# Optimization experiments

Measured on AMD Instinct MI355X. Metric: run time of the kernel, lower is better.

Reference implementation:

```python
import jax, jax.numpy as jnp
import numpy as np

B, S, D, H = 4, 2048, 1024, 16
DK = D // H

def setup_inputs() -> dict:
    key = jax.random.key(0)
    ks = jax.random.split(key, 12)
    def lin(kk, fan_in):
        bound = 1.0 / np.sqrt(fan_in)
        kw, kb = jax.random.split(kk)
        W = jax.random.uniform(kw, (fan_in, D), jnp.float32, -bound, bound)
        b = jax.random.uniform(kb, (D,), jnp.float32, -bound, bound)
        return W, b
    Wq, bq = lin(ks[0], D)
    Wk, bk = lin(ks[1], D)
    Wv, bv = lin(ks[2], D)
    Wo, bo = lin(ks[3], D)
    q = jax.random.normal(ks[4], (B, S, D), jnp.float32)
    k = jax.random.normal(ks[5], (B, S, D), jnp.float32)
    v = jax.random.normal(ks[6], (B, S, D), jnp.float32)
    mask = jnp.tril(jnp.ones((S, S), jnp.int32))[None, None]  # [1,1,S,S] causal
    return {"q": q, "k": k, "v": v, "mask": mask,
            "Wq": Wq, "bq": bq, "Wk": Wk, "bk": bk,
            "Wv": Wv, "bv": bv, "Wo": Wo, "bo": bo}

def reference(q, k, v, mask, Wq, bq, Wk, bk, Wv, bv, Wo, bo):
    Bq, Sq, _ = q.shape
    # projections
    Q = (q @ Wq + bq).reshape(Bq, Sq, H, DK).transpose(0, 2, 1, 3)  # [B,H,S,DK]
    K = (k @ Wk + bk).reshape(Bq, Sq, H, DK).transpose(0, 2, 1, 3)
    V = (v @ Wv + bv).reshape(Bq, Sq, H, DK).transpose(0, 2, 1, 3)
    scale = 1.0 / jnp.sqrt(jnp.float32(DK))
    scores = jnp.einsum('bhqd,bhkd->bhqk', Q, K) * scale  # [B,H,S,S]
    scores = jnp.where(mask == 0, jnp.float32(-jnp.inf), scores)
    attn = jax.nn.softmax(scores, axis=-1)
    # dropout p=0.0 -> identity
    x = jnp.einsum('bhqk,bhkd->bhqd', attn, V)  # [B,H,S,DK]
    x = x.transpose(0, 2, 1, 3).reshape(Bq, Sq, D)
    return x @ Wo + bo
```

## Files before the change

### kernel.cpp

```cpp
#include <hip/hip_runtime.h>

typedef unsigned short u16;
typedef __attribute__((ext_vector_type(4))) float f32x4;
typedef __attribute__((ext_vector_type(8))) __bf16 bf16x8;
typedef __attribute__((ext_vector_type(4))) unsigned int u32x4;

#define S_LEN 2048
#define D_DIM 1024
#define N_HEADS 16
#define DK 64
#define B_SZ 4

__device__ __forceinline__ u16 f2bf(float f) {
  unsigned int u = __float_as_uint(f);
  unsigned int r = (u + 0x7FFFu + ((u >> 16) & 1u)) >> 16;
  return (u16)r;
}
__device__ __forceinline__ unsigned int cvtpk(float a, float b) {
  unsigned int r;
  asm("v_cvt_pk_bf16_f32 %0, %1, %2" : "=v"(r) : "v"(a), "v"(b));
  return r;
}
__device__ __forceinline__ f32x4 mfma16(u32x4 a, u32x4 b, f32x4 c) {
  return __builtin_amdgcn_mfma_f32_16x16x32_bf16(
      __builtin_bit_cast(bf16x8, a), __builtin_bit_cast(bf16x8, b), c, 0, 0, 0);
}
__device__ __forceinline__ void gload_lds16(const void* g, void* l) {
  __builtin_amdgcn_global_load_lds(
      (const __attribute__((address_space(1))) void*)g,
      (__attribute__((address_space(3))) void*)l, 16, 0, 0);
}

__global__ __launch_bounds__(256) void transpose_all(
    const float* __restrict__ W0, const float* __restrict__ W1,
    const float* __restrict__ W2, const float* __restrict__ W3,
    u16* __restrict__ T0, u16* __restrict__ T1,
    u16* __restrict__ T2, u16* __restrict__ T3) {
  __shared__ float tb[32][33];
  const int z = blockIdx.z;
  const float* W = (z == 0) ? W0 : (z == 1) ? W1 : (z == 2) ? W2 : W3;
  u16* WT = (z == 0) ? T0 : (z == 1) ? T1 : (z == 2) ? T2 : T3;
  const int tx = threadIdx.x & 31;
  const int ty0 = (threadIdx.x >> 5) << 2;
  const int bn = blockIdx.x << 5;
  const int bk = blockIdx.y << 5;
#pragma unroll
  for (int i = 0; i < 4; ++i)
    tb[ty0 + i][tx] = W[(size_t)(bk + ty0 + i) * D_DIM + bn + tx];
  __syncthreads();
#pragma unroll
  for (int i = 0; i < 4; ++i)
    WT[(size_t)(bn + ty0 + i) * D_DIM + bk + tx] = f2bf(tb[tx][ty0 + i]);
}

template <int AF32, int BPRE>
__global__ __launch_bounds__(256) void gemm_xw(const void* __restrict__ Av,
                                               const void* __restrict__ Bv,
                                               const float* __restrict__ bias,
                                               void* __restrict__ dstv,
                                               const int epi, const float osc) {
  __shared__ __align__(16) u16 As[128 * 40];
  __shared__ __align__(16) u16 Bs[128 * 40];
  const int tid = threadIdx.x;
  const int lane = tid & 63;
  const int wid = tid >> 6;
  const int wr = wid >> 1, wc = wid & 1;
  const int lr = lane & 15, lg = lane >> 4;
  const int m0 = blockIdx.x * 128;
  const int n0 = blockIdx.y * 128;

  const float* Xf = (const float*)Av;
  const u16* Xh = (const u16*)Av;
  const float* Wf = (const float*)Bv;
  const u16* WT = (const u16*)Bv;

  f32x4 acc[4][4];
#pragma unroll
  for (int i = 0; i < 4; ++i)
#pragma unroll
    for (int j = 0; j < 4; ++j) acc[i][j] = (f32x4){0.f, 0.f, 0.f, 0.f};

  const int srow = tid >> 2;
  const int sko = (tid & 3) << 3;
  const int glr = lane >> 2;
  const int glc = ((lane & 3) ^ (glr & 3)) << 3;

  for (int k0 = 0; k0 < D_DIM; k0 += 32) {
    __syncthreads();
    if (AF32) {
#pragma unroll
      for (int i = 0; i < 2; ++i) {
        const int row = srow + i * 64;
        const float* src = &Xf[(size_t)(m0 + row) * D_DIM + k0 + sko];
        f32x4 a0 = *(const f32x4*)src;
        f32x4 a1 = *(const f32x4*)(src + 4);
        u32x4 pk = (u32x4){cvtpk(a0[0], a0[1]), cvtpk(a0[2], a0[3]),
                           cvtpk(a1[0], a1[1]), cvtpk(a1[2], a1[3])};
        *(u32x4*)&As[row * 40 + sko] = pk;
      }
    } else {
#pragma unroll
      for (int j = 0; j < 2; ++j) {
        const int rbase = wid * 32 + j * 16;
        gload_lds16(&Xh[(size_t)(m0 + rbase + glr) * D_DIM + k0 + glc],
                    &As[rbase * 32]);
      }
    }
    if (BPRE) {
#pragma unroll
      for (int j = 0; j < 2; ++j) {
        const int rbase = wid * 32 + j * 16;
        gload_lds16(&WT[(size_t)(n0 + rbase + glr) * D_DIM + k0 + glc],
                    &Bs[rbase * 32]);
      }
    } else {
#pragma unroll
      for (int i = 0; i < 2; ++i) {
        const int s = tid + (i << 8);
        const int kr = s >> 4;
        const int mN = s & 15;
        const int nc = mN << 3;
        const float* src = &Wf[(size_t)(k0 + kr) * D_DIM + n0 + nc];
        f32x4 w0 = *(const f32x4*)src;
        f32x4 w1 = *(const f32x4*)(src + 4);
        const int cb = (((kr >> 3) ^ (mN & 3)) << 3) + (kr & 7);
#pragma unroll
        for (int j = 0; j < 4; ++j) {
          Bs[(nc + j) * 40 + cb] = f2bf(w0[j]);
          Bs[(nc + 4 + j) * 40 + cb] = f2bf(w1[j]);
        }
      }
    }
    __syncthreads();
    u32x4 af[4], bfr[4];
#pragma unroll
    for (int mi = 0; mi < 4; ++mi) {
      const int row = wr * 64 + mi * 16 + lr;
      if (AF32)
        af[mi] = *(const u32x4*)&As[row * 40 + lg * 8];
      else
        af[mi] = *(const u32x4*)&As[row * 32 + ((lg ^ (row & 3)) << 3)];
    }
#pragma unroll
    for (int ni = 0; ni < 4; ++ni) {
      const int row = wc * 64 + ni * 16 + lr;
      if (BPRE)
        bfr[ni] = *(const u32x4*)&Bs[row * 32 + ((lg ^ (row & 3)) << 3)];
      else
        bfr[ni] = *(const u32x4*)&Bs[row * 40 + ((lg ^ ((row >> 3) & 3)) << 3)];
    }
#pragma unroll
    for (int mi = 0; mi < 4; ++mi)
#pragma unroll
      for (int ni = 0; ni < 4; ++ni)
        acc[mi][ni] = mfma16(af[mi], bfr[ni], acc[mi][ni]);
  }

#pragma unroll
  for (int ni = 0; ni < 4; ++ni) {
    const int n = n0 + wc * 64 + ni * 16 + lr;
    const float bv = bias[n];
#pragma unroll
    for (int mi = 0; mi < 4; ++mi) {
      const int mb = m0 + wr * 64 + mi * 16 + lg * 4;
      float o[4];
#pragma unroll
      for (int r = 0; r < 4; ++r) o[r] = (acc[mi][ni][r] + bv) * osc;
      if (epi == 0) {
#pragma unroll
        for (int r = 0; r < 4; ++r)
          ((float*)dstv)[(size_t)(mb + r) * D_DIM + n] = o[r];
      } else {
        const unsigned int w0 = cvtpk(o[0], o[1]);
        const unsigned int w1 = cvtpk(o[2], o[3]);
        const int bb = mb >> 11, ss = mb & (S_LEN - 1);
        const int hh = n >> 6, dd = n & (DK - 1);
        if (epi == 2) {
          union { unsigned int u[2]; unsigned long long q; } pk;
          pk.u[0] = w0; pk.u[1] = w1;
          *(unsigned long long*)&((u16*)dstv)[((size_t)((bb * N_HEADS + hh) * DK + dd)) * S_LEN + ss] = pk.q;
        } else {
          u16* dp = &((u16*)dstv)[(((size_t)(bb * N_HEADS + hh) * S_LEN) + ss) * DK + dd];
          dp[0] = (u16)w0;
          dp[DK] = (u16)(w0 >> 16);
          dp[2 * DK] = (u16)w1;
          dp[3 * DK] = (u16)(w1 >> 16);
        }
      }
    }
  }
}

__global__ __launch_bounds__(256) void attn_kernel(const u16* __restrict__ Qb,
                                                   const u16* __restrict__ Kb,
                                                   const u16* __restrict__ VTb,
                                                   u16* __restrict__ Xb) {
  __shared__ __align__(16) u16 Vt[2][64 * 64];
  __shared__ __align__(16) u16 Pl[4][32 * 76];

  const int tid = threadIdx.x;
  const int lane = tid & 63;
  const int w = tid >> 6;
  const int lr = lane & 15;
  const int lg = lane >> 4;

  const int id = (int)blockIdx.x;
  const int xcd = id & 7;
  const int slot = id >> 3;
  const int bh_hi = slot & 7;
  const int qpos = slot >> 3;
  const int grp = qpos >> 2, pos = qpos & 3;
  const int qi = (grp == 0) ? pos : (grp == 1) ? (15 - pos)
               : (grp == 2) ? (4 + pos) : (11 - pos);
  const int q0 = qi * 128;
  const int bh = (bh_hi << 3) | xcd;
  const int h = bh & (N_HEADS - 1);
  const int b = bh >> 4;

  const u16* Qh = Qb + ((size_t)bh) * S_LEN * DK;
  const u16* Kh = Kb + ((size_t)bh) * S_LEN * DK;
  const u16* VTh = VTb + ((size_t)bh) * DK * S_LEN;

  const int wrow = q0 + w * 32;
  const int nt = (q0 >> 6) + 2;

  const int vdk = tid >> 3;
  const int vc = tid & 7;

  const u32x4 ONES = {0x3F803F80u, 0x3F803F80u, 0x3F803F80u, 0x3F803F80u};

  u32x4 qf[2][2];
#pragma unroll
  for (int m = 0; m < 2; ++m)
#pragma unroll
    for (int g = 0; g < 2; ++g)
      qf[m][g] = *(const u32x4*)&Qh[(size_t)(wrow + m * 16 + lr) * DK + g * 32 + lg * 8];

  f32x4 xacc[2][4], sacc[2];
#pragma unroll
  for (int m = 0; m < 2; ++m) {
#pragma unroll
    for (int i = 0; i < 4; ++i) xacc[m][i] = (f32x4){0.f, 0.f, 0.f, 0.f};
    sacc[m] = (f32x4){0.f, 0.f, 0.f, 0.f};
  }

  u32x4 vpre[2], kreg[8];
#pragma unroll
  for (int i = 0; i < 2; ++i)
    vpre[i] = *(const u32x4*)&VTh[(size_t)(vdk + i * 32) * S_LEN + vc * 8];
#pragma unroll
  for (int g = 0; g < 2; ++g)
#pragma unroll
    for (int tt = 0; tt < 4; ++tt)
      kreg[g * 4 + tt] = *(const u32x4*)&Kh[(size_t)(tt * 16 + lr) * DK + g * 32 + lg * 8];
#pragma unroll
  for (int i = 0; i < 2; ++i) {
    const int dk = vdk + i * 32;
    *(u32x4*)&Vt[0][dk * 64 + ((vc ^ (dk & 7)) << 3)] = vpre[i];
  }

  for (int t = 0; t < nt; ++t) {
    const int kp0 = t << 6;
    const bool wact = (kp0 <= wrow + 31);
    const bool dmask = (kp0 + 63 > wrow);
    f32x4 sc[2][4];
#pragma unroll
    for (int m = 0; m < 2; ++m)
#pragma unroll
      for (int tt = 0; tt < 4; ++tt) sc[m][tt] = (f32x4){0.f, 0.f, 0.f, 0.f};
    if (wact) {
      __builtin_amdgcn_s_setprio(1);
#pragma unroll
      for (int g = 0; g < 2; ++g)
#pragma unroll
        for (int tt = 0; tt < 4; ++tt) {
          sc[0][tt] = mfma16(kreg[g * 4 + tt], qf[0][g], sc[0][tt]);
          sc[1][tt] = mfma16(kreg[g * 4 + tt], qf[1][g], sc[1][tt]);
        }
      __builtin_amdgcn_s_setprio(0);
#pragma unroll
      for (int m = 0; m < 2; ++m) {
        const int qre = wrow + m * 16 + lr;
        float pv[4][4];
        if (dmask) {
#pragma unroll
          for (int tt = 0; tt < 4; ++tt)
#pragma unroll
            for (int r = 0; r < 4; ++r) {
              const int kpe = kp0 + tt * 16 + lg * 4 + r;
              float s = sc[m][tt][r];
              if (kpe > qre) s = -1e30f;
              pv[tt][r] = exp2f(s);
            }
        } else {
#pragma unroll
          for (int tt = 0; tt < 4; ++tt)
#pragma unroll
            for (int r = 0; r < 4; ++r) pv[tt][r] = exp2f(sc[m][tt][r]);
        }
#pragma unroll
        for (int tt = 0; tt < 4; ++tt) {
          uint2 pw;
          pw.x = cvtpk(pv[tt][0], pv[tt][1]);
          pw.y = cvtpk(pv[tt][2], pv[tt][3]);
          *(uint2*)&Pl[w][(m * 16 + lr) * 76 + tt * 16 + lg * 4] = pw;
        }
      }
    }
    __syncthreads();
    const bool pre = (t + 1 < nt);
    if (pre) {
      const int kn = (t + 1) << 6;
#pragma unroll
      for (int i = 0; i < 2; ++i)
        vpre[i] = *(const u32x4*)&VTh[(size_t)(vdk + i * 32) * S_LEN + kn + vc * 8];
#pragma unroll
      for (int g = 0; g < 2; ++g)
#pragma unroll
        for (int tt = 0; tt < 4; ++tt)
          kreg[g * 4 + tt] = *(const u32x4*)&Kh[(size_t)(kn + tt * 16 + lr) * DK + g * 32 + lg * 8];
    }
    if (wact) {
      u32x4 pf[2][2];
#pragma unroll
      for (int m = 0; m < 2; ++m) {
        pf[m][0] = *(const u32x4*)&Pl[w][(m * 16 + lr) * 76 + lg * 8];
        pf[m][1] = *(const u32x4*)&Pl[w][(m * 16 + lr) * 76 + 32 + lg * 8];
      }
      __builtin_amdgcn_s_setprio(1);
#pragma unroll
      for (int db = 0; db < 4; ++db) {
        const int vr = db * 16 + lr;
        u32x4 vf0 = *(const u32x4*)&Vt[t & 1][vr * 64 + ((lg ^ (vr & 7)) << 3)];
        u32x4 vf1 = *(const u32x4*)&Vt[t & 1][vr * 64 + (((lg ^ 4) ^ (vr & 7)) << 3)];
#pragma unroll
        for (int m = 0; m < 2; ++m) {
          xacc[m][db] = mfma16(pf[m][0], vf0, xacc[m][db]);
          xacc[m][db] = mfma16(pf[m][1], vf1, xacc[m][db]);
        }
      }
#pragma unroll
      for (int m = 0; m < 2; ++m) {
        sacc[m] = mfma16(pf[m][0], ONES, sacc[m]);
        sacc[m] = mfma16(pf[m][1], ONES, sacc[m]);
      }
      __builtin_amdgcn_s_setprio(0);
    }
    if (pre) {
#pragma unroll
      for (int i = 0; i < 2; ++i) {
        const int dk = vdk + i * 32;
        *(u32x4*)&Vt[(t + 1) & 1][dk * 64 + ((vc ^ (dk & 7)) << 3)] = vpre[i];
      }
    }
  }

#pragma unroll
  for (int m = 0; m < 2; ++m)
#pragma unroll
    for (int r = 0; r < 4; ++r) {
      const float inv = 1.0f / fmaxf(sacc[m][r], 1e-30f);
      const int srow = wrow + m * 16 + lg * 4 + r;
      const size_t base = ((size_t)b * S_LEN + srow) * D_DIM + h * DK;
      const unsigned int w0 = cvtpk(xacc[m][0][r] * inv, xacc[m][1][r] * inv);
      const unsigned int w1 = cvtpk(xacc[m][2][r] * inv, xacc[m][3][r] * inv);
      Xb[base + 0 * 16 + lr] = (u16)w0;
      Xb[base + 1 * 16 + lr] = (u16)(w0 >> 16);
      Xb[base + 2 * 16 + lr] = (u16)w1;
      Xb[base + 3 * 16 + lr] = (u16)(w1 >> 16);
    }
}

extern "C" void kernel_launch(void* const* d_in, const int* in_sizes, int n_in,
                              void* d_out, int out_size, void* d_ws, size_t ws_size,
                              hipStream_t stream) {
  const float* q = (const float*)d_in[0];
  const float* k = (const float*)d_in[1];
  const float* v = (const float*)d_in[2];
  const float* Wq = (const float*)d_in[4];  const float* bq = (const float*)d_in[5];
  const float* Wk = (const float*)d_in[6];  const float* bk = (const float*)d_in[7];
  const float* Wv = (const float*)d_in[8];  const float* bv = (const float*)d_in[9];
  const float* Wo = (const float*)d_in[10]; const float* bo = (const float*)d_in[11];

  u16* Qb = (u16*)d_out;
  u16* Kb = Qb + (8u << 20);
  u16* VTb = (u16*)d_ws;
  u16* Xb = VTb + (8u << 20);

  const float scl = 0.125f * 1.4426950408889634f;
  const dim3 tb(256);
  const size_t need = ((size_t)(8u << 20)) * 2 * 2 + 4 * ((size_t)(1u << 20)) * 2;

  if (ws_size >= need) {
    u16* WqT = Xb + (8u << 20);
    u16* WkT = WqT + (1u << 20);
    u16* WvT = WkT + (1u << 20);
    u16* WoT = WvT + (1u << 20);
    transpose_all<<<dim3(32, 32, 4), tb, 0, stream>>>(Wq, Wk, Wv, Wo, WqT, WkT, WvT, WoT);
    gemm_xw<1, 1><<<dim3(64, 8), tb, 0, stream>>>(q, WqT, bq, Qb, 1, scl);
    gemm_xw<1, 1><<<dim3(64, 8), tb, 0, stream>>>(k, WkT, bk, Kb, 1, 1.0f);
    gemm_xw<1, 1><<<dim3(64, 8), tb, 0, stream>>>(v, WvT, bv, VTb, 2, 1.0f);
    attn_kernel<<<dim3(1024), tb, 0, stream>>>(Qb, Kb, VTb, Xb);
    gemm_xw<0, 1><<<dim3(64, 8), tb, 0, stream>>>(Xb, WoT, bo, d_out, 0, 1.0f);
  } else {
    gemm_xw<1, 0><<<dim3(64, 8), tb, 0, stream>>>(q, Wq, bq, Qb, 1, scl);
    gemm_xw<1, 0><<<dim3(64, 8), tb, 0, stream>>>(k, Wk, bk, Kb, 1, 1.0f);
    gemm_xw<1, 0><<<dim3(64, 8), tb, 0, stream>>>(v, Wv, bv, VTb, 2, 1.0f);
    attn_kernel<<<dim3(1024), tb, 0, stream>>>(Qb, Kb, VTb, Xb);
    gemm_xw<0, 0><<<dim3(64, 8), tb, 0, stream>>>(Xb, Wo, bo, d_out, 0, 1.0f);
  }
}
```

Measured before the change: 224.8 us.

## Batch QKV projections into one launch and drop LDS staging of V in attention

The three Q/K/V projection GEMMs become a single launch with a z-dimension that picks the input, weight, bias and epilogue, so one 1536-block grid replaces three 512-block grids. In the attention kernel, V^T fragments are now read straight from global memory into the PV MFMAs instead of being staged through a double-buffered LDS tile. This removes the per-iteration __syncthreads, so each wave runs its own causal range independently, and the K prefetch moves inside the active-wave branch. The cost is extra global/L2 traffic, since each wave reloads V instead of sharing one LDS copy per block, and V loads now sit directly in front of the MFMAs with no prefetch to hide their latency.

```diff
diff --git a/kernel.cpp b/kernel.cpp
--- a/kernel.cpp
+++ b/kernel.cpp
@@ -54,11 +54,12 @@
 }
 
 template <int AF32, int BPRE>
-__global__ __launch_bounds__(256) void gemm_xw(const void* __restrict__ Av,
-                                               const void* __restrict__ Bv,
-                                               const float* __restrict__ bias,
-                                               void* __restrict__ dstv,
-                                               const int epi, const float osc) {
+__device__ __forceinline__ void gemm_body(const void* __restrict__ Av,
+                                          const void* __restrict__ Bv,
+                                          const float* __restrict__ bias,
+                                          void* __restrict__ dstv,
+                                          const int epi, const float osc,
+                                          const int m0, const int n0) {
   __shared__ __align__(16) u16 As[128 * 40];
   __shared__ __align__(16) u16 Bs[128 * 40];
   const int tid = threadIdx.x;
@@ -66,8 +67,6 @@
   const int wid = tid >> 6;
   const int wr = wid >> 1, wc = wid & 1;
   const int lr = lane & 15, lg = lane >> 4;
-  const int m0 = blockIdx.x * 128;
-  const int n0 = blockIdx.y * 128;
 
   const float* Xf = (const float*)Av;
   const u16* Xh = (const u16*)Av;
@@ -191,11 +190,36 @@
   }
 }
 
+template <int AF32, int BPRE>
+__global__ __launch_bounds__(256) void gemm_xw(const void* __restrict__ Av,
+                                               const void* __restrict__ Bv,
+                                               const float* __restrict__ bias,
+                                               void* __restrict__ dstv,
+                                               const int epi, const float osc) {
+  gemm_body<AF32, BPRE>(Av, Bv, bias, dstv, epi, osc,
+                        (int)blockIdx.x * 128, (int)blockIdx.y * 128);
+}
+
+__global__ __launch_bounds__(256) void gemm_qkv(
+    const float* __restrict__ q, const float* __restrict__ k,
+    const float* __restrict__ v, const u16* __restrict__ WqT,
+    const u16* __restrict__ WkT, const u16* __restrict__ WvT,
+    const float* __restrict__ bq, const float* __restrict__ bk,
+    const float* __restrict__ bv, u16* __restrict__ Qb, u16* __restrict__ Kb,
+    u16* __restrict__ VTb, const float scl) {
+  const int z = blockIdx.z;
+  const float* A = (z == 0) ? q : (z == 1) ? k : v;
+  const u16* WT = (z == 0) ? WqT : (z == 1) ? WkT : WvT;
+  const float* bias = (z == 0) ? bq : (z == 1) ? bk : bv;
+  u16* dst = (z == 0) ? Qb : (z == 1) ? Kb : VTb;
+  gemm_body<1, 1>(A, WT, bias, dst, (z == 2) ? 2 : 1, (z == 0) ? scl : 1.0f,
+                  (int)blockIdx.x * 128, (int)blockIdx.y * 128);
+}
+
 __global__ __launch_bounds__(256) void attn_kernel(const u16* __restrict__ Qb,
                                                    const u16* __restrict__ Kb,
                                                    const u16* __restrict__ VTb,
                                                    u16* __restrict__ Xb) {
-  __shared__ __align__(16) u16 Vt[2][64 * 64];
   __shared__ __align__(16) u16 Pl[4][32 * 76];
 
   const int tid = threadIdx.x;
@@ -224,9 +248,6 @@
   const int wrow = q0 + w * 32;
   const int nt = (q0 >> 6) + 2;
 
-  const int vdk = tid >> 3;
-  const int vc = tid & 7;
-
   const u32x4 ONES = {0x3F803F80u, 0x3F803F80u, 0x3F803F80u, 0x3F803F80u};
 
   u32x4 qf[2][2];
@@ -244,31 +265,23 @@
     sacc[m] = (f32x4){0.f, 0.f, 0.f, 0.f};
   }
 
-  u32x4 vpre[2], kreg[8];
-#pragma unroll
-  for (int i = 0; i < 2; ++i)
-    vpre[i] = *(const u32x4*)&VTh[(size_t)(vdk + i * 32) * S_LEN + vc * 8];
+  u32x4 kreg[8];
 #pragma unroll
   for (int g = 0; g < 2; ++g)
 #pragma unroll
     for (int tt = 0; tt < 4; ++tt)
       kreg[g * 4 + tt] = *(const u32x4*)&Kh[(size_t)(tt * 16 + lr) * DK + g * 32 + lg * 8];
-#pragma unroll
-  for (int i = 0; i < 2; ++i) {
-    const int dk = vdk + i * 32;
-    *(u32x4*)&Vt[0][dk * 64 + ((vc ^ (dk & 7)) << 3)] = vpre[i];
-  }
 
   for (int t = 0; t < nt; ++t) {
     const int kp0 = t << 6;
     const bool wact = (kp0 <= wrow + 31);
-    const bool dmask = (kp0 + 63 > wrow);
-    f32x4 sc[2][4];
-#pragma unroll
-    for (int m = 0; m < 2; ++m)
-#pragma unroll
-      for (int tt = 0; tt < 4; ++tt) sc[m][tt] = (f32x4){0.f, 0.f, 0.f, 0.f};
     if (wact) {
+      const bool dmask = (kp0 + 63 > wrow);
+      f32x4 sc[2][4];
+#pragma unroll
+      for (int m = 0; m < 2; ++m)
+#pragma unroll
+        for (int tt = 0; tt < 4; ++tt) sc[m][tt] = (f32x4){0.f, 0.f, 0.f, 0.f};
       __builtin_amdgcn_s_setprio(1);
 #pragma unroll
       for (int g = 0; g < 2; ++g)
@@ -278,6 +291,14 @@
           sc[1][tt] = mfma16(kreg[g * 4 + tt], qf[1][g], sc[1][tt]);
         }
       __builtin_amdgcn_s_setprio(0);
+      if (t + 1 < nt) {
+        const int kn = (t + 1) << 6;
+#pragma unroll
+        for (int g = 0; g < 2; ++g)
+#pragma unroll
+          for (int tt = 0; tt < 4; ++tt)
+            kreg[g * 4 + tt] = *(const u32x4*)&Kh[(size_t)(kn + tt * 16 + lr) * DK + g * 32 + lg * 8];
+      }
 #pragma unroll
       for (int m = 0; m < 2; ++m) {
         const int qre = wrow + m * 16 + lr;
@@ -306,21 +327,6 @@
           *(uint2*)&Pl[w][(m * 16 + lr) * 76 + tt * 16 + lg * 4] = pw;
         }
       }
-    }
-    __syncthreads();
-    const bool pre = (t + 1 < nt);
-    if (pre) {
-      const int kn = (t + 1) << 6;
-#pragma unroll
-      for (int i = 0; i < 2; ++i)
-        vpre[i] = *(const u32x4*)&VTh[(size_t)(vdk + i * 32) * S_LEN + kn + vc * 8];
-#pragma unroll
-      for (int g = 0; g < 2; ++g)
-#pragma unroll
-        for (int tt = 0; tt < 4; ++tt)
-          kreg[g * 4 + tt] = *(const u32x4*)&Kh[(size_t)(kn + tt * 16 + lr) * DK + g * 32 + lg * 8];
-    }
-    if (wact) {
       u32x4 pf[2][2];
 #pragma unroll
       for (int m = 0; m < 2; ++m) {
@@ -330,13 +336,12 @@
       __builtin_amdgcn_s_setprio(1);
 #pragma unroll
       for (int db = 0; db < 4; ++db) {
-        const int vr = db * 16 + lr;
-        u32x4 vf0 = *(const u32x4*)&Vt[t & 1][vr * 64 + ((lg ^ (vr & 7)) << 3)];
-        u32x4 vf1 = *(const u32x4*)&Vt[t & 1][vr * 64 + (((lg ^ 4) ^ (vr & 7)) << 3)];
-#pragma unroll
-        for (int m = 0; m < 2; ++m) {
-          xacc[m][db] = mfma16(pf[m][0], vf0, xacc[m][db]);
-          xacc[m][db] = mfma16(pf[m][1], vf1, xacc[m][db]);
+#pragma unroll
+        for (int g = 0; g < 2; ++g) {
+          u32x4 vf = *(const u32x4*)&VTh[(size_t)(db * 16 + lr) * S_LEN + kp0 + g * 32 + lg * 8];
+#pragma unroll
+          for (int m = 0; m < 2; ++m)
+            xacc[m][db] = mfma16(pf[m][g], vf, xacc[m][db]);
         }
       }
 #pragma unroll
@@ -345,13 +350,6 @@
         sacc[m] = mfma16(pf[m][1], ONES, sacc[m]);
       }
       __builtin_amdgcn_s_setprio(0);
-    }
-    if (pre) {
-#pragma unroll
-      for (int i = 0; i < 2; ++i) {
-        const int dk = vdk + i * 32;
-        *(u32x4*)&Vt[(t + 1) & 1][dk * 64 + ((vc ^ (dk & 7)) << 3)] = vpre[i];
-      }
     }
   }
 
@@ -397,9 +395,8 @@
     u16* WvT = WkT + (1u << 20);
     u16* WoT = WvT + (1u << 20);
     transpose_all<<<dim3(32, 32, 4), tb, 0, stream>>>(Wq, Wk, Wv, Wo, WqT, WkT, WvT, WoT);
-    gemm_xw<1, 1><<<dim3(64, 8), tb, 0, stream>>>(q, WqT, bq, Qb, 1, scl);
-    gemm_xw<1, 1><<<dim3(64, 8), tb, 0, stream>>>(k, WkT, bk, Kb, 1, 1.0f);
-    gemm_xw<1, 1><<<dim3(64, 8), tb, 0, stream>>>(v, WvT, bv, VTb, 2, 1.0f);
+    gemm_qkv<<<dim3(64, 8, 3), tb, 0, stream>>>(q, k, v, WqT, WkT, WvT,
+                                                bq, bk, bv, Qb, Kb, VTb, scl);
     attn_kernel<<<dim3(1024), tb, 0, stream>>>(Qb, Kb, VTb, Xb);
     gemm_xw<0, 1><<<dim3(64, 8), tb, 0, stream>>>(Xb, WoT, bo, d_out, 0, 1.0f);
   } else {
```

Result: slower. 250.7 us (+11.5%).
